# Optimization experiments

Measured on AMD Instinct MI355X. Metric: run time of the kernel, lower is better.

Reference implementation:

```python
import jax, jax.numpy as jnp
import numpy as np

B, TIN, TOUT = 128, 512, 64
IN_F, OUT_F, H = 64, 32, 1024
DEC_IN = IN_F + OUT_F  # decoder GRU input size


def setup_inputs() -> dict:
    key = jax.random.key(0)
    ks = jax.random.split(key, 24)
    s = 1.0 / np.sqrt(H)
    u = lambda k, shp: jax.random.uniform(k, shp, jnp.float32, -s, s)
    return {
        "enc_input": jax.random.normal(ks[0], (B, TIN, IN_F), jnp.float32),
        "dec_input": jax.random.normal(ks[1], (B, TOUT, IN_F), jnp.float32),
        # encoder GRU, layer 0 (input IN_F) and layer 1 (input H); gates stacked [r,z,n]
        "enc_Wih0": u(ks[2], (3 * H, IN_F)), "enc_Whh0": u(ks[3], (3 * H, H)),
        "enc_bih0": u(ks[4], (3 * H,)), "enc_bhh0": u(ks[5], (3 * H,)),
        "enc_Wih1": u(ks[6], (3 * H, H)), "enc_Whh1": u(ks[7], (3 * H, H)),
        "enc_bih1": u(ks[8], (3 * H,)), "enc_bhh1": u(ks[9], (3 * H,)),
        # decoder GRU, layer 0 (input DEC_IN) and layer 1 (input H)
        "dec_Wih0": u(ks[10], (3 * H, DEC_IN)), "dec_Whh0": u(ks[11], (3 * H, H)),
        "dec_bih0": u(ks[12], (3 * H,)), "dec_bhh0": u(ks[13], (3 * H,)),
        "dec_Wih1": u(ks[14], (3 * H, H)), "dec_Whh1": u(ks[15], (3 * H, H)),
        "dec_bih1": u(ks[16], (3 * H,)), "dec_bhh1": u(ks[17], (3 * H,)),
        # output MLP: Linear(H,H)+ReLU, then Linear(H,OUT_F, bias=False)
        "out1_W": u(ks[18], (H, H)), "out1_b": u(ks[19], (H,)),
        "out2_W": u(ks[20], (OUT_F, H)),
    }


def _gru_cell(x, h, Wih, Whh, bih, bhh):
    """Single GRU step, PyTorch gate convention. x:(B,in) h:(B,H) -> (B,H)."""
    gi = x @ Wih.T + bih
    gh = h @ Whh.T + bhh
    ir, iz, inn = jnp.split(gi, 3, axis=-1)
    hr, hz, hn = jnp.split(gh, 3, axis=-1)
    r = jax.nn.sigmoid(ir + hr)
    z = jax.nn.sigmoid(iz + hz)
    n = jnp.tanh(inn + r * hn)
    return (1.0 - z) * n + z * h


def _gru_layer(x, h0, Wih, Whh, bih, bhh):
    """Full-sequence GRU layer. x:(B,T,in) -> (ys:(B,T,H), hT:(B,H))."""
    xp = jnp.einsum('bti,gi->btg', x, Wih) + bih  # precompute input projections
    def step(h, g):
        gh = h @ Whh.T + bhh
        ir, iz, inn = jnp.split(g, 3, axis=-1)
        hr, hz, hn = jnp.split(gh, 3, axis=-1)
        r = jax.nn.sigmoid(ir + hr)
        z = jax.nn.sigmoid(iz + hz)
        n = jnp.tanh(inn + r * hn)
        hnew = (1.0 - z) * n + z * h
        return hnew, hnew
    hT, ys = jax.lax.scan(step, h0, jnp.swapaxes(xp, 0, 1))
    return jnp.swapaxes(ys, 0, 1), hT


def _forward(enc_input, dec_input,
             enc_Wih0, enc_Whh0, enc_bih0, enc_bhh0,
             enc_Wih1, enc_Whh1, enc_bih1, enc_bhh1,
             dec_Wih0, dec_Whh0, dec_bih0, dec_bhh0,
             dec_Wih1, dec_Whh1, dec_bih1, dec_bhh1,
             out1_W, out1_b, out2_W):
    b = enc_input.shape[0]
    zeros = jnp.zeros((b, H), enc_input.dtype)
    # encoder: 2-layer GRU from zero state
    y0, eh0 = _gru_layer(enc_input, zeros, enc_Wih0, enc_Whh0, enc_bih0, enc_bhh0)
    _, eh1 = _gru_layer(y0, zeros, enc_Wih1, enc_Whh1, enc_bih1, enc_bhh1)
    y_prev0 = enc_input[:, -1, :OUT_F]
    def dec_step(carry, x_t):
        y_prev, h0, h1 = carry
        x = jnp.concatenate([y_prev, x_t], axis=-1)  # (B, OUT_F+IN_F)
        h0n = _gru_cell(x, h0, dec_Wih0, dec_Whh0, dec_bih0, dec_bhh0)
        h1n = _gru_cell(h0n, h1, dec_Wih1, dec_Whh1, dec_bih1, dec_bhh1)
        out = jax.nn.relu(h1n @ out1_W.T + out1_b) @ out2_W.T  # dropout=identity (eval)
        return (out, h0n, h1n), out
    _, ys = jax.lax.scan(dec_step, (y_prev0, eh0, eh1), jnp.swapaxes(dec_input, 0, 1))
    return jnp.swapaxes(ys, 0, 1)  # (B, TOUT, OUT_F)


def reference(enc_input, dec_input,
              enc_Wih0, enc_Whh0, enc_bih0, enc_bhh0,
              enc_Wih1, enc_Whh1, enc_bih1, enc_bhh1,
              dec_Wih0, dec_Whh0, dec_bih0, dec_bhh0,
              dec_Wih1, dec_Whh1, dec_bih1, dec_bhh1,
              out1_W, out1_b, out2_W):
    return _forward(enc_input, dec_input,
                    enc_Wih0, enc_Whh0, enc_bih0, enc_bhh0,
                    enc_Wih1, enc_Whh1, enc_bih1, enc_bhh1,
                    dec_Wih0, dec_Whh0, dec_bih0, dec_bhh0,
                    dec_Wih1, dec_Whh1, dec_bih1, dec_bhh1,
                    out1_W, out1_b, out2_W)
```

## Files before the change

### kernel.cpp

```cpp
#include <hip/hip_runtime.h>

typedef unsigned short u16;
typedef unsigned long long u64;
typedef __attribute__((ext_vector_type(8))) short bf16x8;
typedef __attribute__((ext_vector_type(4))) float f32x4;

#define Bsz   128
#define TIN   512
#define TOUT  64
#define INF   64
#define OUTF  32
#define Hdim  1024
#define H3    3072

#define K0    1088
#define K1    2048
#define KD0   1120
#define KD1   2048
#define KH    1024

#define SX0  (Bsz * K0)
#define SX1  (Bsz * K1)
#define SXD0 (Bsz * KD0)
#define SXD1 (Bsz * KD1)
#define SH   (Bsz * Hdim)

#define BAR_ROOT 512
#define BAR_GEN  528
#define GRP_BASE 1024
#define BAR_WORDS 2048

__device__ __forceinline__ u16 f2bf(float f) {
    union { float f; unsigned u; } c; c.f = f;
    unsigned u = c.u;
    unsigned r = (u + 0x7fffu + ((u >> 16) & 1u)) >> 16;
    return (u16)r;
}

__device__ __forceinline__ f32x4 mfma16(bf16x8 a, bf16x8 b, f32x4 c) {
    return __builtin_amdgcn_mfma_f32_16x16x32_bf16(a, b, c, 0, 0, 0);
}

__device__ __forceinline__ void tile_map32(int wg, int& htile, int& bq) {
    const int xcd = wg & 7, idx = wg >> 3;
    htile = ((idx & 3) << 3) + xcd;
    bq = idx >> 2;
}

__device__ __forceinline__ u64 ald64(const void* p) {
    return __hip_atomic_load((const u64*)p, __ATOMIC_RELAXED, __HIP_MEMORY_SCOPE_AGENT);
}
__device__ __forceinline__ void ast64(void* p, u64 v) {
    __hip_atomic_store((u64*)p, v, __ATOMIC_RELAXED, __HIP_MEMORY_SCOPE_AGENT);
}
__device__ __forceinline__ float aldf(const float* p) {
    return __hip_atomic_load(p, __ATOMIC_RELAXED, __HIP_MEMORY_SCOPE_AGENT);
}
__device__ __forceinline__ void astf(float* p, float v) {
    __hip_atomic_store(p, v, __ATOMIC_RELAXED, __HIP_MEMORY_SCOPE_AGENT);
}
__device__ __forceinline__ u16 aldu16(const u16* p) {
    return __hip_atomic_load(p, __ATOMIC_RELAXED, __HIP_MEMORY_SCOPE_AGENT);
}
__device__ __forceinline__ void astu16(u16* p, u16 v) {
    __hip_atomic_store(p, v, __ATOMIC_RELAXED, __HIP_MEMORY_SCOPE_AGENT);
}
__device__ __forceinline__ bf16x8 ldx(const u16* p) {
    union { u64 q[2]; bf16x8 v; } u;
    u.q[0] = ald64(p);
    u.q[1] = ald64(p + 4);
    return u.v;
}

__device__ __forceinline__ void ldg16_nt(const u16* p, bf16x8& v) {
    asm volatile("global_load_dwordx4 %0, %1, off sc0 sc1 nt"
                 : "=&v"(v) : "v"(p));
}

template <unsigned NB>
__device__ __forceinline__ void groupbar(unsigned* arr, unsigned* gen, unsigned target) {
    __syncthreads();
    if (threadIdx.x == 0) {
        asm volatile("s_waitcnt vmcnt(0) lgkmcnt(0)" ::: "memory");
        unsigned a = __hip_atomic_fetch_add(arr, 1u,
                        __ATOMIC_RELAXED, __HIP_MEMORY_SCOPE_AGENT);
        if (((a + 1u) & (NB - 1u)) == 0u)
            __hip_atomic_fetch_add(gen, 1u,
                        __ATOMIC_RELAXED, __HIP_MEMORY_SCOPE_AGENT);
        while (__hip_atomic_load(gen, __ATOMIC_RELAXED, __HIP_MEMORY_SCOPE_AGENT) < target)
            __builtin_amdgcn_s_sleep(2);
        asm volatile("" ::: "memory");
    }
    __syncthreads();
}

__device__ __forceinline__ void waitgen(unsigned* gen, unsigned target) {
    if (threadIdx.x == 0) {
        while (__hip_atomic_load(gen, __ATOMIC_RELAXED, __HIP_MEMORY_SCOPE_AGENT) < target)
            __builtin_amdgcn_s_sleep(2);
        asm volatile("" ::: "memory");
    }
    __syncthreads();
}

__device__ __forceinline__ void gridbar(unsigned* bar, unsigned target) {
    __syncthreads();
    if (threadIdx.x == 0) {
        asm volatile("s_waitcnt vmcnt(0) lgkmcnt(0)" ::: "memory");
        unsigned leaf = (blockIdx.x >> 3) << 4;
        unsigned a = __hip_atomic_fetch_add(&bar[leaf], 1u,
                        __ATOMIC_RELAXED, __HIP_MEMORY_SCOPE_AGENT);
        if (((a + 1u) & 7u) == 0u) {
            unsigned r = __hip_atomic_fetch_add(&bar[BAR_ROOT], 1u,
                            __ATOMIC_RELAXED, __HIP_MEMORY_SCOPE_AGENT);
            if (((r + 1u) & 31u) == 0u)
                __hip_atomic_fetch_add(&bar[BAR_GEN], 1u,
                        __ATOMIC_RELAXED, __HIP_MEMORY_SCOPE_AGENT);
        }
        while (__hip_atomic_load(&bar[BAR_GEN],
                    __ATOMIC_RELAXED, __HIP_MEMORY_SCOPE_AGENT) < target)
            __builtin_amdgcn_s_sleep(2);
        asm volatile("" ::: "memory");
    }
    __syncthreads();
}

__device__ __forceinline__ unsigned* grp_arr(unsigned* bar, int g) { return bar + GRP_BASE + g * 32; }
__device__ __forceinline__ unsigned* grp_gen(unsigned* bar, int g) { return bar + GRP_BASE + g * 32 + 16; }


__global__ void __launch_bounds__(256) pack2(
        const float* __restrict__ A, int KA,
        const float* __restrict__ Bs, int KB,
        u16* __restrict__ dst) {
    int row = blockIdx.y;
    int k = blockIdx.x * 256 + threadIdx.x;
    int K = KA + KB;
    if (k >= K) return;
    float v = (k < KA) ? A[(size_t)row * KA + k] : Bs[(size_t)row * KB + (k - KA)];
    dst[(size_t)row * K + k] = f2bf(v);
}

__global__ void __launch_bounds__(256) pack_bias(
        const float* bi0e, const float* bh0e,
        const float* bi1e, const float* bh1e,
        const float* bi0d, const float* bh0d,
        const float* bi1d, const float* bh1d,
        const float* out1b,
        float* B0, float* B1, float* BD0, float* BD1, float* HB) {
    int j = blockIdx.x * blockDim.x + threadIdx.x;
    if (j >= 1024) return;
    const float* bis[4] = { bi0e, bi1e, bi0d, bi1d };
    const float* bhs[4] = { bh0e, bh1e, bh0d, bh1d };
    float* ds[4] = { B0, B1, BD0, BD1 };
#pragma unroll
    for (int s = 0; s < 4; ++s) {
        ds[s][j]        = bis[s][j]        + bhs[s][j];
        ds[s][1024 + j] = bis[s][1024 + j] + bhs[s][1024 + j];
        ds[s][2048 + j] = bis[s][2048 + j];
        ds[s][3072 + j] = bhs[s][2048 + j];
    }
    HB[j] = out1b[j];
}

__global__ void __launch_bounds__(256) init_state(
        const float* __restrict__ enc_input,
        u16* __restrict__ X0, u16* __restrict__ X1,
        float* __restrict__ H0f, float* __restrict__ H1f,
        unsigned* __restrict__ bar) {
    int gtid = blockIdx.x * blockDim.x + threadIdx.x;
    int G = gridDim.x * blockDim.x;
    for (int i = gtid; i < BAR_WORDS; i += G) bar[i] = 0u;
    for (int i = gtid; i < Bsz * Hdim; i += G) { int b = i >> 10, j = i & 1023; X0[(size_t)b * K0 + j] = 0; }
    for (int i = gtid; i < Bsz * INF; i += G) { int b = i >> 6, f = i & 63;
        X0[(size_t)b * K0 + 1024 + f] = f2bf(enc_input[(size_t)b * (TIN * INF) + f]); }
    for (int i = gtid; i < Bsz * Hdim; i += G) { int b = i >> 10, j = i & 1023;
        X1[(size_t)SX1 + (size_t)b * K1 + j] = 0; }
    for (int i = gtid; i < Bsz * Hdim; i += G) { H0f[i] = 0.f; H1f[SH + i] = 0.f; }
}

template <int K>
__device__ __forceinline__ void stage_x(const u16* __restrict__ Xsrc, u16* __restrict__ xl) {
    const int tid = threadIdx.x;
    const int r = tid >> 4, tj = tid & 15;
    const u16* srow = Xsrc + (size_t)r * K;
    const unsigned base = (unsigned)(r * K * 2);
    const unsigned swz = (unsigned)((r & 7) << 4);
    constexpr int U = K / 8;
    for (int k0 = tj; k0 < U; k0 += 128) {
        bf16x8 t[8];
#pragma unroll
        for (int i = 0; i < 8; ++i) {
            int k = k0 + i * 16;
            if (k < U) ldg16_nt(srow + k * 8, t[i]);
        }
        asm volatile("s_waitcnt vmcnt(0)" ::: "memory");
        __builtin_amdgcn_sched_barrier(0);
#pragma unroll
        for (int i = 0; i < 8; ++i) {
            int k = k0 + i * 16;
            if (k < U)
                *(bf16x8*)((char*)xl + ((base + (unsigned)k * 16u) ^ swz)) = t[i];
        }
    }
}

template <int KB0, int KB1, int SPLIT, int K>
__device__ __forceinline__ void gru_wave_lds(
        const u16* __restrict__ W, const u16* __restrict__ xl,
        int j0w, int row,
        f32x4& accR, f32x4& accZ, f32x4& accN0, f32x4& accN1) {
    const int lane = threadIdx.x & 63;
    const int l15 = lane & 15, kq = lane >> 4;
    const u16* Wr = W + (size_t)(j0w + l15) * K + kq * 8;
    const u16* Wz = Wr + (size_t)1024 * K;
    const u16* Wn = Wz + (size_t)1024 * K;
    const unsigned xbase = (unsigned)(row * K * 2 + kq * 16);
    const unsigned swz = (unsigned)((row & 7) << 4);
    accR = (f32x4){0.f, 0.f, 0.f, 0.f};
    accZ = (f32x4){0.f, 0.f, 0.f, 0.f};
    accN0 = (f32x4){0.f, 0.f, 0.f, 0.f};
    accN1 = (f32x4){0.f, 0.f, 0.f, 0.f};
    constexpr int E0 = (SPLIT < KB1) ? SPLIT : KB1;
    constexpr int S1 = (SPLIT > KB0) ? SPLIT : KB0;
#pragma unroll 8
    for (int kb = KB0; kb < E0; ++kb) {
        const int o = kb * 32;
        bf16x8 xb = *(const bf16x8*)((const char*)xl + ((xbase + (unsigned)kb * 64u) ^ swz));
        accR  = mfma16(*(const bf16x8*)(Wr + o), xb, accR);
        accZ  = mfma16(*(const bf16x8*)(Wz + o), xb, accZ);
        accN0 = mfma16(*(const bf16x8*)(Wn + o), xb, accN0);
    }
#pragma unroll 8
    for (int kb = S1; kb < KB1; ++kb) {
        const int o = kb * 32;
        bf16x8 xb = *(const bf16x8*)((const char*)xl + ((xbase + (unsigned)kb * 64u) ^ swz));
        accR  = mfma16(*(const bf16x8*)(Wr + o), xb, accR);
        accZ  = mfma16(*(const bf16x8*)(Wz + o), xb, accZ);
        accN1 = mfma16(*(const bf16x8*)(Wn + o), xb, accN1);
    }
}

template <int KBT, int SPLIT, int K>
__device__ __forceinline__ void gru_block32(
        const u16* __restrict__ W, const u16* __restrict__ X,
        const float* __restrict__ Hold, const float* __restrict__ Bias,
        int htile, int bq,
        float* __restrict__ Hnew,
        u16* __restrict__ O1, int ld1, int off1,
        u16* __restrict__ O2, int ld2, int off2,
        float* __restrict__ sred , u16* __restrict__ xl) {
    stage_x<K>(X + (size_t)bq * 32 * K, xl);
    __syncthreads();

    const int tid = threadIdx.x, lane = tid & 63, w = tid >> 6;
    const int hf = w & 1, bf = (w >> 1) & 1, grp = w >> 2, bg = w & 3;
    const int l15 = lane & 15, kq = lane >> 4;
    const int j0w = htile * 32 + hf * 16;
    const int rowl = bf * 16 + l15;
    constexpr int MID = KBT / 2;

    f32x4 aR, aZ, aN0, aN1;
    if (grp == 0) gru_wave_lds<0, MID, SPLIT, K>(W, xl, j0w, rowl, aR, aZ, aN0, aN1);
    else          gru_wave_lds<MID, KBT, SPLIT, K>(W, xl, j0w, rowl, aR, aZ, aN0, aN1);

    float* slot = sred + ((size_t)bg * 64 + lane) * 17;
    if (grp == 1) {
#pragma unroll
        for (int q = 0; q < 4; ++q) {
            slot[q]      = aR[q];
            slot[4 + q]  = aZ[q];
            slot[8 + q]  = aN0[q];
            slot[12 + q] = aN1[q];
        }
    }
    __syncthreads();
    if (grp == 0) {
        const int nb = bq * 32 + bf * 16 + l15;
        float hv4[4];
#pragma unroll
        for (int q = 0; q < 4; ++q) {
            const int j = j0w + kq * 4 + q;
            float R  = aR[q]  + slot[q];
            float Z  = aZ[q]  + slot[4 + q];
            float Nh = aN0[q] + slot[8 + q];
            float Ni = aN1[q] + slot[12 + q];
            float r = 1.f / (1.f + expf(-(R + Bias[j])));
            float z = 1.f / (1.f + expf(-(Z + Bias[1024 + j])));
            float n = tanhf(Ni + Bias[2048 + j] + r * (Nh + Bias[3072 + j]));
            float ho = aldf(&Hold[(size_t)j * Bsz + nb]);
            float hv = (1.f - z) * n + z * ho;
            astf(&Hnew[(size_t)j * Bsz + nb], hv);
            hv4[q] = hv;
        }
        union { u16 h[4]; u64 q8; } pk;
#pragma unroll
        for (int q = 0; q < 4; ++q) pk.h[q] = f2bf(hv4[q]);
        ast64(&O1[(size_t)nb * ld1 + off1 + j0w + kq * 4], pk.q8);
        if (O2) ast64(&O2[(size_t)nb * ld2 + off2 + j0w + kq * 4], pk.q8);
    }
}

struct KParams {
    const float* enc_input;
    const float* dec_input;
    const u16 *W0, *W1, *WD0, *WD1, *WH1, *WH2;
    const float *B0, *B1, *BD0, *BD1, *HB;
    u16 *X0, *X1, *XD0, *XD1, *Hhead, *Abuf;
    float *H0f, *H1f;
    float* out;
    unsigned* bar;
};


__device__ __forceinline__ void enc_L0_round(const KParams& p, int r, int htile, int bq,
                                             float* sred, u16* xl) {
    const int pr = r & 1, pw = pr ^ 1;
    gru_block32<34, 32, K0>(p.W0, p.X0 + pr * SX0, p.H0f + pr * SH, p.B0,
                            htile, bq,
                            p.H0f + pw * SH,
                            p.X0 + pw * SX0, K0, 0,
                            p.X1 + pw * SX1, K1, 1024, sred, xl);
    if (r + 1 < 512 && threadIdx.x < 16) {
        int b = bq * 32 + htile, f4 = threadIdx.x * 4;
        const float* src = p.enc_input + ((size_t)b * TIN + (r + 1)) * INF + f4;
        union { u16 h[4]; u64 q8; } pk;
#pragma unroll
        for (int i = 0; i < 4; ++i) pk.h[i] = f2bf(src[i]);
        ast64(&p.X0[(size_t)pw * SX0 + (size_t)b * K0 + 1024 + f4], pk.q8);
    }
}

__device__ __forceinline__ void enc_L1_step(const KParams& p, int s, int htile, int bq,
                                            float* sred, u16* xl) {
    const int pr = s & 1, pw = pr ^ 1;
    gru_block32<64, 32, K1>(p.W1, p.X1 + pr * SX1, p.H1f + pr * SH, p.B1,
                            htile, bq,
                            p.H1f + pw * SH,
                            p.X1 + pw * SX1, K1, 0,
                            (u16*)nullptr, 0, 0, sred, xl);
}

__device__ __forceinline__ void transition_body(const KParams& p) {
    int gtid = blockIdx.x * blockDim.x + threadIdx.x;
    const int G = 256 * 512;
    for (int i = gtid; i < SH; i += G)
        astf(&p.H1f[i], aldf(&p.H1f[SH + i]));
    for (int i = gtid; i < Bsz * Hdim; i += G) {
        int b = i >> 10, j = i & 1023;
        astu16(&p.XD0[(size_t)b * KD0 + j], aldu16(&p.X0[(size_t)b * K0 + j]));
    }
    for (int i = gtid; i < Bsz * OUTF; i += G) {
        int b = i >> 5, f = i & 31;
        astu16(&p.XD0[(size_t)b * KD0 + 1024 + f],
               f2bf(p.enc_input[((size_t)b * TIN + (TIN - 1)) * INF + f]));
    }
    for (int i = gtid; i < Bsz * INF; i += G) {
        int b = i >> 6, f = i & 63;
        astu16(&p.XD0[(size_t)b * KD0 + 1056 + f],
               f2bf(p.dec_input[(size_t)b * (TOUT * INF) + f]));
    }
    for (int i = gtid; i < Bsz * Hdim; i += G) {
        int b = i >> 10, j = i & 1023;
        astu16(&p.XD1[(size_t)b * KD1 + j],
               aldu16(&p.X1[(size_t)SX1 + (size_t)b * K1 + j]));
    }
}

__device__ __forceinline__ void dec_A_body(const KParams& p, int t, int htile, int bq,
                                           float* sred, u16* xl) {
    const int pt = t & 1, pn = pt ^ 1;
    gru_block32<35, 32, KD0>(p.WD0, p.XD0 + pt * SXD0, p.H0f + pt * SH, p.BD0,
                             htile, bq,
                             p.H0f + pn * SH,
                             p.XD0 + pn * SXD0, KD0, 0,
                             p.XD1 + pt * SXD1, KD1, 1024, sred, xl);
}

__device__ __forceinline__ void dec_B_body(const KParams& p, int t, int htile, int bq,
                                           float* sred, u16* xl) {
    const int pt = t & 1, pn = pt ^ 1;
    gru_block32<64, 32, KD1>(p.WD1, p.XD1 + pt * SXD1, p.H1f + pt * SH, p.BD1,
                             htile, bq,
                             p.H1f + pn * SH,
                             p.XD1 + pn * SXD1, KD1, 0,
                             p.Hhead, KH, 0, sred, xl);
}

__device__ __forceinline__ void dec_C_body(const KParams& p, int t, int htile, int bq,
                                           float* sred, u16* xl) {
    const int pn = (t & 1) ^ 1;
    stage_x<KH>(p.Hhead + (size_t)bq * 32 * KH, xl);
    __syncthreads();

    const int tid = threadIdx.x, lane = tid & 63, w = tid >> 6;
    const int hf = w & 1, bf = (w >> 1) & 1, grp = w >> 2, bg = w & 3;
    const int l15 = lane & 15, kq = lane >> 4;
    const int j0w = htile * 32 + hf * 16;
    const int rowl = bf * 16 + l15;

    const u16* Wr = p.WH1 + (size_t)(j0w + l15) * KH + kq * 8;
    const unsigned xbase = (unsigned)(rowl * KH * 2 + kq * 16);
    const unsigned swz = (unsigned)((rowl & 7) << 4);
    f32x4 acc = {0.f, 0.f, 0.f, 0.f};
    const int kb0 = grp * 16, kb1 = kb0 + 16;
#pragma unroll 8
    for (int kb = kb0; kb < kb1; ++kb) {
        bf16x8 xb = *(const bf16x8*)((const char*)xl + ((xbase + (unsigned)kb * 64u) ^ swz));
        acc = mfma16(*(const bf16x8*)(Wr + kb * 32), xb, acc);
    }
    float* slot = sred + ((size_t)bg * 64 + lane) * 17;
    if (grp == 1) {
#pragma unroll
        for (int q = 0; q < 4; ++q) slot[q] = acc[q];
    }
    __syncthreads();
    if (grp == 0) {
        const int nb = bq * 32 + bf * 16 + l15;
        union { u16 h[4]; u64 q8; } pk;
#pragma unroll
        for (int q = 0; q < 4; ++q) {
            const int j = j0w + kq * 4 + q;
            float v = acc[q] + slot[q] + p.HB[j];
            pk.h[q] = f2bf(v > 0.f ? v : 0.f);
        }
        ast64(&p.Abuf[(size_t)nb * KH + j0w + kq * 4], pk.q8);
    }
    if (t + 1 < TOUT && tid < 16) {
        int b = bq * 32 + htile, f4 = tid * 4;
        const float* src = p.dec_input + ((size_t)b * TOUT + (t + 1)) * INF + f4;
        union { u16 h[4]; u64 q8; } pk2;
#pragma unroll
        for (int i = 0; i < 4; ++i) pk2.h[i] = f2bf(src[i]);
        ast64(&p.XD0[(size_t)pn * SXD0 + (size_t)b * KD0 + 1056 + f4], pk2.q8);
    }
}

__device__ __forceinline__ void dec_D_body(const KParams& p, int t, int htile, int bq,
                                           float* sred) {
    const int pn = (t & 1) ^ 1;
    const int tid = threadIdx.x, lane = tid & 63, w = tid >> 6;
    const int l15 = lane & 15, kq = lane >> 4;
    const int mt = htile & 1, ntl = htile >> 1;
    const int brow = bq * 32 + ntl * 16;
    if (w < 4) {
        const u16* Wr = p.WH2 + (size_t)(mt * 16 + l15) * KH + kq * 8;
        const u16* Xb = p.Abuf + (size_t)(brow + l15) * KH + kq * 8;
        f32x4 acc = {0.f, 0.f, 0.f, 0.f};
#pragma unroll 8
        for (int kb = w * 8; kb < w * 8 + 8; ++kb) {
            const int o = kb * 32;
            acc = mfma16(*(const bf16x8*)(Wr + o), ldx(Xb + o), acc);
        }
#pragma unroll
        for (int q = 0; q < 4; ++q) sred[(w * 64 + lane) * 4 + q] = acc[q];
    }
    __syncthreads();
    if (w == 0) {
        int b = brow + l15;
        union { u16 h[4]; u64 q8; } pk;
#pragma unroll
        for (int q = 0; q < 4; ++q) {
            float s = sred[(0 * 64 + lane) * 4 + q] + sred[(1 * 64 + lane) * 4 + q] +
                      sred[(2 * 64 + lane) * 4 + q] + sred[(3 * 64 + lane) * 4 + q];
            int feat = mt * 16 + kq * 4 + q;
            p.out[(size_t)b * (TOUT * OUTF) + t * OUTF + feat] = s;
            pk.h[q] = f2bf(s);
        }
        ast64(&p.XD0[(size_t)pn * SXD0 + (size_t)b * KD0 + 1024 + mt * 16 + kq * 4], pk.q8);
    }
}

__global__ void __launch_bounds__(512, 1) seq2seq_persist(KParams p) {
    __shared__ float sred[4 * 64 * 17];
    __shared__ u16 xls[32 * 2048];
    unsigned* bar = p.bar;
    const int wg = blockIdx.x;

    if (wg < 128) {
        int htile, bq; tile_map32(wg, htile, bq);
        unsigned* arrL0 = grp_arr(bar, bq);
        unsigned* genL0 = grp_gen(bar, bq);
        unsigned* genL1 = grp_gen(bar, 4 + bq);
        for (int r = 0; r < 512; ++r) {
            if (r >= 2) waitgen(genL1, (unsigned)(r - 1));
            enc_L0_round(p, r, htile, bq, sred, xls);
            groupbar<32>(arrL0, genL0, (unsigned)(r + 1));
        }
    } else {
        int htile, bq; tile_map32(wg - 128, htile, bq);
        unsigned* arrL1 = grp_arr(bar, 4 + bq);
        unsigned* genL1 = grp_gen(bar, 4 + bq);
        unsigned* genL0 = grp_gen(bar, bq);
        for (int s = 1; s <= 512; ++s) {
            waitgen(genL0, (unsigned)s);
            enc_L1_step(p, s, htile, bq, sred, xls);
            groupbar<32>(arrL1, genL1, (unsigned)s);
        }
    }

    gridbar(bar, 1);
    transition_body(p);
    gridbar(bar, 2);

    if (wg < 128) {
        int htile, bq; tile_map32(wg, htile, bq);
        unsigned* arrA = grp_arr(bar, 8 + bq);  unsigned* genA = grp_gen(bar, 8 + bq);
        unsigned* arrB = grp_arr(bar, 12 + bq); unsigned* genB = grp_gen(bar, 12 + bq);
        unsigned* arrC = grp_arr(bar, 16 + bq); unsigned* genC = grp_gen(bar, 16 + bq);
        unsigned* arrD = grp_arr(bar, 20 + bq); unsigned* genD = grp_gen(bar, 20 + bq);
        for (int t = 0; t < TOUT; ++t) {
            if (t >= 1) waitgen(genD, (unsigned)t);
            dec_A_body(p, t, htile, bq, sred, xls);
            groupbar<32>(arrA, genA, (unsigned)(t + 1));
            dec_B_body(p, t, htile, bq, sred, xls);
            groupbar<32>(arrB, genB, (unsigned)(t + 1));
            dec_C_body(p, t, htile, bq, sred, xls);
            groupbar<32>(arrC, genC, (unsigned)(t + 1));
            if (htile < 4) {
                dec_D_body(p, t, htile, bq, sred);
                groupbar<4>(arrD, genD, (unsigned)(t + 1));
            }
        }
    }
}

extern "C" void kernel_launch(void* const* d_in, const int* in_sizes, int n_in,
                              void* d_out, int out_size, void* d_ws, size_t ws_size,
                              hipStream_t stream) {
    const float* enc_input = (const float*)d_in[0];
    const float* dec_input = (const float*)d_in[1];
    const float* enc_Wih0 = (const float*)d_in[2];
    const float* enc_Whh0 = (const float*)d_in[3];
    const float* enc_bih0 = (const float*)d_in[4];
    const float* enc_bhh0 = (const float*)d_in[5];
    const float* enc_Wih1 = (const float*)d_in[6];
    const float* enc_Whh1 = (const float*)d_in[7];
    const float* enc_bih1 = (const float*)d_in[8];
    const float* enc_bhh1 = (const float*)d_in[9];
    const float* dec_Wih0 = (const float*)d_in[10];
    const float* dec_Whh0 = (const float*)d_in[11];
    const float* dec_bih0 = (const float*)d_in[12];
    const float* dec_bhh0 = (const float*)d_in[13];
    const float* dec_Wih1 = (const float*)d_in[14];
    const float* dec_Whh1 = (const float*)d_in[15];
    const float* dec_bih1 = (const float*)d_in[16];
    const float* dec_bhh1 = (const float*)d_in[17];
    const float* out1_W = (const float*)d_in[18];
    const float* out1_b = (const float*)d_in[19];
    const float* out2_W = (const float*)d_in[20];

    char* ws = (char*)d_ws;
    size_t off = 0;
    auto alloc = [&](size_t bytes) { size_t o = off; off = (off + bytes + 255) & ~(size_t)255; return o; };

    u16* W0 = (u16*)(ws + alloc((size_t)H3 * K0 * 2));
    u16* W1 = (u16*)(ws + alloc((size_t)H3 * K1 * 2));
    u16* WD0 = (u16*)(ws + alloc((size_t)H3 * KD0 * 2));
    u16* WD1 = (u16*)(ws + alloc((size_t)H3 * KD1 * 2));
    u16* WH1 = (u16*)(ws + alloc((size_t)Hdim * KH * 2));
    u16* WH2 = (u16*)(ws + alloc((size_t)OUTF * KH * 2));
    float* B0 = (float*)(ws + alloc(4096 * 4));
    float* B1 = (float*)(ws + alloc(4096 * 4));
    float* BD0 = (float*)(ws + alloc(4096 * 4));
    float* BD1 = (float*)(ws + alloc(4096 * 4));
    float* HB = (float*)(ws + alloc(1024 * 4));
    u16* X0 = (u16*)(ws + alloc((size_t)2 * Bsz * K0 * 2));
    u16* X1 = (u16*)(ws + alloc((size_t)2 * Bsz * K1 * 2));
    u16* XD0 = (u16*)(ws + alloc((size_t)2 * Bsz * KD0 * 2));
    u16* XD1 = (u16*)(ws + alloc((size_t)2 * Bsz * KD1 * 2));
    float* H0f = (float*)(ws + alloc((size_t)2 * Bsz * Hdim * 4));
    float* H1f = (float*)(ws + alloc((size_t)2 * Bsz * Hdim * 4));
    u16* Hhead = (u16*)(ws + alloc((size_t)Bsz * KH * 2));
    u16* Abuf = (u16*)(ws + alloc((size_t)Bsz * KH * 2));
    unsigned* bar = (unsigned*)(ws + alloc(BAR_WORDS * 4));

    pack2<<<dim3((K0 + 255) / 256, H3), 256, 0, stream>>>(enc_Whh0, 1024, enc_Wih0, 64, W0);
    pack2<<<dim3((K1 + 255) / 256, H3), 256, 0, stream>>>(enc_Whh1, 1024, enc_Wih1, 1024, W1);
    pack2<<<dim3((KD0 + 255) / 256, H3), 256, 0, stream>>>(dec_Whh0, 1024, dec_Wih0, 96, WD0);
    pack2<<<dim3((KD1 + 255) / 256, H3), 256, 0, stream>>>(dec_Whh1, 1024, dec_Wih1, 1024, WD1);
    pack2<<<dim3((KH + 255) / 256, Hdim), 256, 0, stream>>>(out1_W, 1024, nullptr, 0, WH1);
    pack2<<<dim3((KH + 255) / 256, OUTF), 256, 0, stream>>>(out2_W, 1024, nullptr, 0, WH2);
    pack_bias<<<4, 256, 0, stream>>>(enc_bih0, enc_bhh0, enc_bih1, enc_bhh1,
                                     dec_bih0, dec_bhh0, dec_bih1, dec_bhh1,
                                     out1_b, B0, B1, BD0, BD1, HB);
    init_state<<<256, 256, 0, stream>>>(enc_input, X0, X1, H0f, H1f, bar);

    KParams kp;
    kp.enc_input = enc_input; kp.dec_input = dec_input;
    kp.W0 = W0; kp.W1 = W1; kp.WD0 = WD0; kp.WD1 = WD1; kp.WH1 = WH1; kp.WH2 = WH2;
    kp.B0 = B0; kp.B1 = B1; kp.BD0 = BD0; kp.BD1 = BD1; kp.HB = HB;
    kp.X0 = X0; kp.X1 = X1; kp.XD0 = XD0; kp.XD1 = XD1; kp.Hhead = Hhead; kp.Abuf = Abuf;
    kp.H0f = H0f; kp.H1f = H1f;
    kp.out = (float*)d_out;
    kp.bar = bar;

    seq2seq_persist<<<256, 512, 0, stream>>>(kp);
}
```

Before: 21.76 ms.

## Pre-tile packed GRU and head weights for contiguous per-wave MFMA loads

Adds a pack_tiled kernel that reorders the bf16 weight matrices into a per-(htile, kb, hf, gate, lane) layout, so each wave's MFMA operand fetch for one k-block is a single contiguous 1KB chunk. Previously each lane read 16 bytes from rows strided by K, touching many cache lines per instruction. The GRU and decoder head loops now index the tiled buffers with simple per-kb offsets. This adds a more complex index computation to the one-time pack kernels and ties the layout to fixed tile constants.

```diff
diff --git a/kernel.cpp b/kernel.cpp
--- a/kernel.cpp
+++ b/kernel.cpp
@@ -128,6 +128,29 @@
 __device__ __forceinline__ unsigned* grp_arr(unsigned* bar, int g) { return bar + GRP_BASE + g * 32; }
 __device__ __forceinline__ unsigned* grp_gen(unsigned* bar, int g) { return bar + GRP_BASE + g * 32 + 16; }
 
+
+__global__ void __launch_bounds__(256) pack_tiled(
+        const float* __restrict__ A, int KA,
+        const float* __restrict__ Bs, int KB,
+        u16* __restrict__ dst, int KBT, int G) {
+    long idx = (long)blockIdx.x * 256 + threadIdx.x;
+    long total = (long)32 * KBT * 2 * G * 512;
+    if (idx >= total) return;
+    int e = (int)(idx & 7);
+    int lane = (int)((idx >> 3) & 63);
+    long r1 = idx >> 9;
+    int g = (int)(r1 % G);
+    long r2 = r1 / G;
+    int hf = (int)(r2 & 1);
+    long r3 = r2 >> 1;
+    int kb = (int)(r3 % KBT);
+    int htile = (int)(r3 / KBT);
+    int row = g * 1024 + htile * 32 + hf * 16 + (lane & 15);
+    int col = kb * 32 + (lane >> 4) * 8 + e;
+    float v = (col < KA) ? A[(size_t)row * KA + col]
+                         : Bs[(size_t)row * KB + (col - KA)];
+    dst[idx] = f2bf(v);
+}
 
 __global__ void __launch_bounds__(256) pack2(
         const float* __restrict__ A, int KA,
@@ -205,16 +228,14 @@
     }
 }
 
-template <int KB0, int KB1, int SPLIT, int K>
+template <int KB0, int KB1, int SPLIT, int K, int KBT>
 __device__ __forceinline__ void gru_wave_lds(
         const u16* __restrict__ W, const u16* __restrict__ xl,
-        int j0w, int row,
+        int htile, int hf, int row,
         f32x4& accR, f32x4& accZ, f32x4& accN0, f32x4& accN1) {
     const int lane = threadIdx.x & 63;
-    const int l15 = lane & 15, kq = lane >> 4;
-    const u16* Wr = W + (size_t)(j0w + l15) * K + kq * 8;
-    const u16* Wz = Wr + (size_t)1024 * K;
-    const u16* Wn = Wz + (size_t)1024 * K;
+    const int kq = lane >> 4;
+    const u16* Wl = W + (size_t)htile * KBT * 3072 + hf * 1536 + lane * 8;
     const unsigned xbase = (unsigned)(row * K * 2 + kq * 16);
     const unsigned swz = (unsigned)((row & 7) << 4);
     accR = (f32x4){0.f, 0.f, 0.f, 0.f};
@@ -225,19 +246,19 @@
     constexpr int S1 = (SPLIT > KB0) ? SPLIT : KB0;
 #pragma unroll 8
     for (int kb = KB0; kb < E0; ++kb) {
-        const int o = kb * 32;
+        const u16* wk = Wl + (size_t)kb * 3072;
         bf16x8 xb = *(const bf16x8*)((const char*)xl + ((xbase + (unsigned)kb * 64u) ^ swz));
-        accR  = mfma16(*(const bf16x8*)(Wr + o), xb, accR);
-        accZ  = mfma16(*(const bf16x8*)(Wz + o), xb, accZ);
-        accN0 = mfma16(*(const bf16x8*)(Wn + o), xb, accN0);
+        accR  = mfma16(*(const bf16x8*)(wk), xb, accR);
+        accZ  = mfma16(*(const bf16x8*)(wk + 512), xb, accZ);
+        accN0 = mfma16(*(const bf16x8*)(wk + 1024), xb, accN0);
     }
 #pragma unroll 8
     for (int kb = S1; kb < KB1; ++kb) {
-        const int o = kb * 32;
+        const u16* wk = Wl + (size_t)kb * 3072;
         bf16x8 xb = *(const bf16x8*)((const char*)xl + ((xbase + (unsigned)kb * 64u) ^ swz));
-        accR  = mfma16(*(const bf16x8*)(Wr + o), xb, accR);
-        accZ  = mfma16(*(const bf16x8*)(Wz + o), xb, accZ);
-        accN1 = mfma16(*(const bf16x8*)(Wn + o), xb, accN1);
+        accR  = mfma16(*(const bf16x8*)(wk), xb, accR);
+        accZ  = mfma16(*(const bf16x8*)(wk + 512), xb, accZ);
+        accN1 = mfma16(*(const bf16x8*)(wk + 1024), xb, accN1);
     }
 }
 
@@ -258,11 +279,10 @@
     const int l15 = lane & 15, kq = lane >> 4;
     const int j0w = htile * 32 + hf * 16;
     const int rowl = bf * 16 + l15;
-    constexpr int MID = KBT / 2;
 
     f32x4 aR, aZ, aN0, aN1;
-    if (grp == 0) gru_wave_lds<0, MID, SPLIT, K>(W, xl, j0w, rowl, aR, aZ, aN0, aN1);
-    else          gru_wave_lds<MID, KBT, SPLIT, K>(W, xl, j0w, rowl, aR, aZ, aN0, aN1);
+    if (grp == 0) gru_wave_lds<0, KBT / 2, SPLIT, K, KBT>(W, xl, htile, hf, rowl, aR, aZ, aN0, aN1);
+    else          gru_wave_lds<KBT / 2, KBT, SPLIT, K, KBT>(W, xl, htile, hf, rowl, aR, aZ, aN0, aN1);
 
     float* slot = sred + ((size_t)bg * 64 + lane) * 17;
     if (grp == 1) {
@@ -399,7 +419,7 @@
     const int j0w = htile * 32 + hf * 16;
     const int rowl = bf * 16 + l15;
 
-    const u16* Wr = p.WH1 + (size_t)(j0w + l15) * KH + kq * 8;
+    const u16* Wl = p.WH1 + (size_t)htile * 32768 + hf * 512 + lane * 8;
     const unsigned xbase = (unsigned)(rowl * KH * 2 + kq * 16);
     const unsigned swz = (unsigned)((rowl & 7) << 4);
     f32x4 acc = {0.f, 0.f, 0.f, 0.f};
@@ -407,7 +427,7 @@
 #pragma unroll 8
     for (int kb = kb0; kb < kb1; ++kb) {
         bf16x8 xb = *(const bf16x8*)((const char*)xl + ((xbase + (unsigned)kb * 64u) ^ swz));
-        acc = mfma16(*(const bf16x8*)(Wr + kb * 32), xb, acc);
+        acc = mfma16(*(const bf16x8*)(Wl + (size_t)kb * 1024), xb, acc);
     }
     float* slot = sred + ((size_t)bg * 64 + lane) * 17;
     if (grp == 1) {
@@ -575,11 +595,12 @@
     u16* Abuf = (u16*)(ws + alloc((size_t)Bsz * KH * 2));
     unsigned* bar = (unsigned*)(ws + alloc(BAR_WORDS * 4));
 
-    pack2<<<dim3((K0 + 255) / 256, H3), 256, 0, stream>>>(enc_Whh0, 1024, enc_Wih0, 64, W0);
-    pack2<<<dim3((K1 + 255) / 256, H3), 256, 0, stream>>>(enc_Whh1, 1024, enc_Wih1, 1024, W1);
-    pack2<<<dim3((KD0 + 255) / 256, H3), 256, 0, stream>>>(dec_Whh0, 1024, dec_Wih0, 96, WD0);
-    pack2<<<dim3((KD1 + 255) / 256, H3), 256, 0, stream>>>(dec_Whh1, 1024, dec_Wih1, 1024, WD1);
-    pack2<<<dim3((KH + 255) / 256, Hdim), 256, 0, stream>>>(out1_W, 1024, nullptr, 0, WH1);
+    auto nblk = [](long total) { return (unsigned)((total + 255) / 256); };
+    pack_tiled<<<nblk((long)32 * 34 * 2 * 3 * 512), 256, 0, stream>>>(enc_Whh0, 1024, enc_Wih0, 64, W0, 34, 3);
+    pack_tiled<<<nblk((long)32 * 64 * 2 * 3 * 512), 256, 0, stream>>>(enc_Whh1, 1024, enc_Whh1 ? enc_Wih1 : nullptr, 1024, W1, 64, 3);
+    pack_tiled<<<nblk((long)32 * 35 * 2 * 3 * 512), 256, 0, stream>>>(dec_Whh0, 1024, dec_Wih0, 96, WD0, 35, 3);
+    pack_tiled<<<nblk((long)32 * 64 * 2 * 3 * 512), 256, 0, stream>>>(dec_Whh1, 1024, dec_Wih1, 1024, WD1, 64, 3);
+    pack_tiled<<<nblk((long)32 * 32 * 2 * 1 * 512), 256, 0, stream>>>(out1_W, 1024, nullptr, 0, WH1, 32, 1);
     pack2<<<dim3((KH + 255) / 256, OUTF), 256, 0, stream>>>(out2_W, 1024, nullptr, 0, WH2);
     pack_bias<<<4, 256, 0, stream>>>(enc_bih0, enc_bhh0, enc_bih1, enc_bhh1,
                                      dec_bih0, dec_bhh0, dec_bih1, dec_bhh1,
```

Measured after the change: 21.70 ms. No clear change (-0.3%).
